# Optimization experiments

Hardware: AMD Instinct MI355X
Metric: run time of the kernel (lower is better)

## Reference

```python
import jax, jax.numpy as jnp
import numpy as np

N = 50000      # num_nodes
E = 500000     # num_edges
D_IN = 128     # in_features
D_OUT = 128    # out_features
D_REL = 128    # nrela_dim
NEG_SLOPE = 0.2   # LeakyReLU alpha
RATIO = 0.5       # float ratio -> simple (non-schedule) branch
LN_EPS = 1e-5


def setup_inputs() -> dict:
    key = jax.random.key(0)
    ks = jax.random.split(key, 8)
    edge_index = jax.random.randint(ks[0], (2, E), 0, N, dtype=jnp.int64)
    x = jax.random.normal(ks[1], (N, D_IN), dtype=jnp.float32)
    edge_type_embed = jax.random.normal(ks[2], (E, D_REL), dtype=jnp.float32)
    # learned params (xavier-ish scale)
    W = jax.random.normal(ks[3], (4, 2 * D_OUT + D_REL, D_OUT), dtype=jnp.float32) * 0.05
    a = jax.random.normal(ks[4], (4, D_OUT, 1), dtype=jnp.float32) * 0.05
    xw = jax.random.normal(ks[5], (D_IN, D_OUT), dtype=jnp.float32) * (1.0 / np.sqrt(D_IN))
    xb = jnp.zeros((D_OUT,), dtype=jnp.float32)
    gamma = jnp.ones((D_OUT,), dtype=jnp.float32)
    beta = jnp.zeros((D_OUT,), dtype=jnp.float32)
    return {"edge_index": edge_index, "x": x, "edge_type_embed": edge_type_embed,
            "W": W, "a": a, "xw": xw, "xb": xb, "gamma": gamma, "beta": beta}


def _segment_softmax(score, seg, num_segments):
    # per-source-node softmax over edges (matches torch_geometric softmax util)
    seg_max = jax.ops.segment_max(score, seg, num_segments=num_segments)
    seg_max = jnp.where(jnp.isfinite(seg_max), seg_max, 0.0)  # empty segments
    e = jnp.exp(score - seg_max[seg])
    denom = jax.ops.segment_sum(e, seg, num_segments=num_segments)
    return e / (denom[seg] + 1e-16)


def _one_iter(edge_index, xc, ete, Wi, ai):
    src, dst = edge_index[0], edge_index[1]
    # [E, 2*D_OUT + D_REL] @ [2*D_OUT+D_REL, D_OUT] -> [E, D_OUT]
    edge_h = jnp.concatenate([xc[src], xc[dst], ete], axis=1) @ Wi
    score = jax.nn.leaky_relu(jnp.squeeze(edge_h @ ai, -1), NEG_SLOPE)  # [E]
    alpha = _segment_softmax(score, src, N)
    k = int(E * RATIO)
    _, idx = jax.lax.top_k(alpha, k)
    mask = jnp.zeros((E,), dtype=bool).at[idx].set(True)
    alpha = jnp.where(mask, alpha, 0.0)
    # scatter-add weighted messages back to source nodes
    return jax.ops.segment_sum(alpha[:, None] * edge_h, src, num_segments=N)


def reference(edge_index, x, edge_type_embed, W, a, xw, xb, gamma, beta):
    xc = x @ xw + xb  # x_linear
    for i in range(4):  # fixed 4 aggregation iterations (float-ratio branch)
        xc = _one_iter(edge_index, xc, edge_type_embed, W[i], a[i])
    xc = jax.nn.elu(xc)  # concat=True
    mu = jnp.mean(xc, axis=-1, keepdims=True)
    var = jnp.var(xc, axis=-1, keepdims=True)
    return (xc - mu) * jax.lax.rsqrt(var + LN_EPS) * gamma + beta
```

## Files before the change

### kernel.cpp

```cpp
#include <hip/hip_runtime.h>
#include <math.h>

#define DOUT 128

typedef unsigned short u16;
typedef __attribute__((ext_vector_type(8))) short bf16x8;
typedef __attribute__((ext_vector_type(4))) float f32x4;

static __device__ __forceinline__ f32x4 mfma16x16x32(bf16x8 a, bf16x8 b, f32x4 c) {
  return __builtin_amdgcn_mfma_f32_16x16x32_bf16(a, b, c, 0, 0, 0);
}

static __device__ __forceinline__ short bf16i(int v) {
  return (short)(__float_as_uint((float)v) >> 16);
}

static __device__ __forceinline__ float wsum64(float v) {
#pragma unroll
  for (int off = 32; off > 0; off >>= 1) v += __shfl_xor(v, off, 64);
  return v;
}
static __device__ __forceinline__ float wmax64(float v) {
#pragma unroll
  for (int off = 32; off > 0; off >>= 1) v = fmaxf(v, __shfl_xor(v, off, 64));
  return v;
}
static __device__ __forceinline__ float rsumg(float v) {
  v += __shfl_xor(v, 16, 64);
  v += __shfl_xor(v, 32, 64);
  return v;
}

static __device__ __forceinline__ void split3(float x, u16& h, u16& m, u16& l) {
  unsigned u = __float_as_uint(x);
  unsigned rh = u + 0x7FFFu + ((u >> 16) & 1u);
  h = (u16)(rh >> 16);
  float hf = __uint_as_float(rh & 0xFFFF0000u);
  float d1 = x - hf;
  unsigned v = __float_as_uint(d1);
  unsigned rm = v + 0x7FFFu + ((v >> 16) & 1u);
  m = (u16)(rm >> 16);
  float mf = __uint_as_float(rm & 0xFFFF0000u);
  float d2 = d1 - mf;
  unsigned w2 = __float_as_uint(d2);
  unsigned rl = w2 + 0x7FFFu + ((w2 >> 16) & 1u);
  l = (u16)(rl >> 16);
}

static __device__ __forceinline__ void split3pk(float x0, float x1,
                                                unsigned& h, unsigned& m, unsigned& l) {
  unsigned hp, mp, lp;
  asm("v_cvt_pk_bf16_f32 %0, %1, %2" : "=v"(hp) : "v"(x0), "v"(x1));
  float d0 = x0 - __uint_as_float(hp << 16);
  float d1 = x1 - __uint_as_float(hp & 0xFFFF0000u);
  asm("v_cvt_pk_bf16_f32 %0, %1, %2" : "=v"(mp) : "v"(d0), "v"(d1));
  float e0 = d0 - __uint_as_float(mp << 16);
  float e1 = d1 - __uint_as_float(mp & 0xFFFF0000u);
  asm("v_cvt_pk_bf16_f32 %0, %1, %2" : "=v"(lp) : "v"(e0), "v"(e1));
  h = hp; m = mp; l = lp;
}
static __device__ __forceinline__ void split34pk(float4 v, uint2& h, uint2& m, uint2& lo) {
  split3pk(v.x, v.y, h.x, m.x, lo.x);
  split3pk(v.z, v.w, h.y, m.y, lo.y);
}

__global__ void zero_detect_kernel(int* __restrict__ degcur, unsigned* __restrict__ hists,
                                   unsigned* __restrict__ rep, int* __restrict__ candcnt4,
                                   int N, const void* __restrict__ ei, int* __restrict__ flag,
                                   int E) {
  int i = blockIdx.x * blockDim.x + threadIdx.x;
  if (i < N) degcur[i] = 0;
  if (i < 4096) hists[i] = 0u;
  if (i < 32768) rep[i] = 0u;
  if (i < 4) candcnt4[i] = 0;
  const int* p = (const int*)ei;
  int lim = (E < 65536) ? E : 65536;
  int any = 0;
  for (int j = i; j < lim; j += gridDim.x * blockDim.x) any |= (p[2 * j + 1] != 0);
  if (__any(any))
    if ((threadIdx.x & 63) == 0 && any) atomicOr(flag, 1);
}

__global__ void cvt_deg_kernel(const void* __restrict__ ei, const int* __restrict__ flag,
                               int* __restrict__ src, int* __restrict__ dst,
                               int* __restrict__ degcur, int E) {
  int i = blockIdx.x * blockDim.x + threadIdx.x;
  if (i >= E) return;
  int s, d;
  if (*flag) { const int* p = (const int*)ei; s = p[i]; d = p[E + i]; }
  else { const long long* p = (const long long*)ei; s = (int)p[i]; d = (int)p[(size_t)E + i]; }
  src[i] = s;
  dst[i] = d;
  atomicAdd(&degcur[s], 1);
}

__global__ void scan_rowptr_kernel(int* __restrict__ degcur, int* __restrict__ rowptr, int N) {
  const int tid = threadIdx.x;
  const int lane = tid & 63, wid = tid >> 6;
  __shared__ int wsumS[16];
  __shared__ int sbase;
  if (tid == 0) sbase = 0;
  __syncthreads();
  for (int base = 0; base < N; base += 1024) {
    int i = base + tid;
    int v = (i < N) ? degcur[i] : 0;
    int x = v;
#pragma unroll
    for (int off = 1; off < 64; off <<= 1) {
      int y = __shfl_up(x, off, 64);
      if (lane >= off) x += y;
    }
    if (lane == 63) wsumS[wid] = x;
    __syncthreads();
    int wbase = 0;
#pragma unroll
    for (int w2 = 0; w2 < 16; ++w2) wbase += (w2 < wid) ? wsumS[w2] : 0;
    int excl = sbase + wbase + x - v;
    if (i < N) { rowptr[i] = excl; degcur[i] = excl; }
    __syncthreads();
    if (tid == 1023) sbase += wbase + x;
    __syncthreads();
  }
  if (tid == 0) rowptr[N] = sbase;
}

__global__ void scatter_kernel(const int* __restrict__ src, int* __restrict__ cursor,
                               int* __restrict__ eids, int E) {
  int e = blockIdx.x * blockDim.x + threadIdx.x;
  if (e >= E) return;
  int p = atomicAdd(&cursor[src[e]], 1);
  eids[p] = e;
}

__global__ void sort_eids_kernel(const int* __restrict__ rowptr, int* __restrict__ eids, int N) {
  int n = blockIdx.x * blockDim.x + threadIdx.x;
  if (n >= N) return;
  int p0 = rowptr[n], p1 = rowptr[n + 1];
  for (int i = p0 + 1; i < p1; ++i) {
    int key = eids[i];
    int j = i - 1;
    while (j >= p0 && eids[j] > key) { eids[j + 1] = eids[j]; --j; }
    eids[j + 1] = key;
  }
}

__global__ void wprep_kernel(const float* __restrict__ W, const float* __restrict__ a,
                             float* __restrict__ wa_all, const float* __restrict__ xw,
                             u16* __restrict__ wtH, u16* __restrict__ wtM,
                             u16* __restrict__ wtL) {
  int blk = blockIdx.x;
  int tid = threadIdx.x;
  if (blk < 4) {
    int it = blk, k = tid;
    const float* row = W + ((size_t)it * 384 + k) * DOUT;
    const float* ai = a + (size_t)it * DOUT;
    float acc = 0.f;
    for (int j = 0; j < DOUT; ++j) acc = fmaf(row[j], ai[j], acc);
    wa_all[it * 384 + k] = acc;
    return;
  }
  __shared__ int muS[32];
  {
    int lw = tid & 63, g = lw >> 4;
    bf16x8 aEnc;
#pragma unroll
    for (int j = 0; j < 8; ++j) aEnc[j] = bf16i(8 * g + j + 1);
    f32x4 z = {0.f, 0.f, 0.f, 0.f};
    for (int t0 = 0; t0 < 32; ++t0) {
      int g0 = t0 >> 3, j0 = t0 & 7;
      bf16x8 bOne;
#pragma unroll
      for (int j = 0; j < 8; ++j)
        bOne[j] = (g == g0 && j == j0) ? (short)0x3F80 : (short)0;
      f32x4 d = mfma16x16x32(aEnc, bOne, z);
      if (tid == t0) muS[t0] = ((int)(d[0] + 0.5f) - 1) & 31;
    }
  }
  __syncthreads();
  int b = blk - 4;
  int set, ks;
  const float* srcp;
  if (b < 4) { set = 0; ks = b; srcp = xw; }
  else { set = 1 + (b - 4) / 12; ks = (b - 4) % 12; srcp = W + (size_t)(set - 1) * 384 * DOUT; }
  size_t base = ((size_t)set * 12 + ks) * 4096;
  for (int i = tid; i < 4096; i += blockDim.x) {
    int col = i >> 5, t = i & 31;
    float x = srcp[(size_t)(ks * 32 + muS[t]) * DOUT + col];
    u16 h, m, l;
    split3(x, h, m, l);
    wtH[base + i] = h;
    wtM[base + i] = m;
    wtL[base + i] = l;
  }
}

__global__ __launch_bounds__(256) void et4_kernel(const float* __restrict__ ete,
                                                  const float* __restrict__ wa_all,
                                                  float* __restrict__ et4, int E) {
  __shared__ float4 w3s[4][32];
  int tid = threadIdx.x;
  if (tid < 128) {
    int it = tid >> 5, k4 = tid & 31;
    const float* base = wa_all + it * 384 + 256 + k4 * 4;
    w3s[it][k4] = make_float4(base[0], base[1], base[2], base[3]);
  }
  __syncthreads();
  int e = blockIdx.x * blockDim.x + tid;
  if (e >= E) return;
  const float4* row = (const float4*)(ete + (size_t)e * DOUT);
  float a0 = 0.f, a1 = 0.f, a2 = 0.f, a3 = 0.f;
#pragma unroll
  for (int k4 = 0; k4 < 32; ++k4) {
    float4 r = row[k4];
    float4 w0 = w3s[0][k4], w1 = w3s[1][k4], w2 = w3s[2][k4], w3v = w3s[3][k4];
    a0 = fmaf(r.x, w0.x, fmaf(r.y, w0.y, fmaf(r.z, w0.z, fmaf(r.w, w0.w, a0))));
    a1 = fmaf(r.x, w1.x, fmaf(r.y, w1.y, fmaf(r.z, w1.z, fmaf(r.w, w1.w, a1))));
    a2 = fmaf(r.x, w2.x, fmaf(r.y, w2.y, fmaf(r.z, w2.z, fmaf(r.w, w2.w, a2))));
    a3 = fmaf(r.x, w3v.x, fmaf(r.y, w3v.y, fmaf(r.z, w3v.z, fmaf(r.w, w3v.w, a3))));
  }
  et4[e] = a0;
  et4[(size_t)E + e] = a1;
  et4[(size_t)2 * E + e] = a2;
  et4[(size_t)3 * E + e] = a3;
}

__global__ __launch_bounds__(256) void softmax_kernel(
    const int* __restrict__ rowptr, const int* __restrict__ eids, const int* __restrict__ dst,
    const float* __restrict__ pa, const float* __restrict__ qa, const float* __restrict__ et4,
    int it, int E, float* __restrict__ alpha, unsigned* __restrict__ rep0, int N) {
  __shared__ unsigned lh[256];
  int tid = threadIdx.x;
  lh[tid] = 0u;
  __syncthreads();
  const float* etp = et4 + (size_t)it * E;
  int w = (int)(((size_t)blockIdx.x * blockDim.x + tid) >> 6);
  int lane = tid & 63;
  if (w < N) {
    int p0 = rowptr[w], p1 = rowptr[w + 1];
    int deg = p1 - p0;
    if (deg > 0) {
      float pan = pa[w];
      if (deg <= 64) {
        int p = p0 + lane;
        int e = -1;
        float sv = -3.402823466e38f;
        if (p < p1) {
          e = eids[p];
          float s = pan + qa[dst[e]] + etp[e];
          sv = (s >= 0.f) ? s : 0.2f * s;
        }
        float m = wmax64(sv);
        float ee = (e >= 0) ? expf(sv - m) : 0.f;
        float den = 0.f;
        for (int i = 0; i < deg; ++i) den += __shfl(ee, i, 64);
        den += 1e-16f;
        if (e >= 0) {
          float av = ee / den;
          alpha[e] = av;
          atomicAdd(&lh[__float_as_uint(av) >> 24], 1u);
        }
      } else if (deg <= 256) {
        float sv[4]; int ev[4];
#pragma unroll
        for (int u = 0; u < 4; ++u) {
          int p = p0 + u * 64 + lane;
          if (p < p1) {
            int e = eids[p];
            ev[u] = e;
            float s = pan + qa[dst[e]] + etp[e];
            sv[u] = (s >= 0.f) ? s : 0.2f * s;
          } else { ev[u] = -1; sv[u] = -3.402823466e38f; }
        }
        float m = fmaxf(fmaxf(sv[0], sv[1]), fmaxf(sv[2], sv[3]));
        m = wmax64(m);
        float ssum = 0.f;
#pragma unroll
        for (int u = 0; u < 4; ++u)
          if (ev[u] >= 0) { sv[u] = expf(sv[u] - m); ssum += sv[u]; }
        ssum = wsum64(ssum);
        float den = ssum + 1e-16f;
#pragma unroll
        for (int u = 0; u < 4; ++u)
          if (ev[u] >= 0) {
            float av = sv[u] / den;
            alpha[ev[u]] = av;
            atomicAdd(&lh[__float_as_uint(av) >> 24], 1u);
          }
      } else {
        float m = -3.402823466e38f;
        for (int p = p0 + lane; p < p1; p += 64) {
          int e = eids[p];
          float s = pan + qa[dst[e]] + etp[e];
          s = (s >= 0.f) ? s : 0.2f * s;
          m = fmaxf(m, s);
        }
        m = wmax64(m);
        float ssum = 0.f;
        for (int p = p0 + lane; p < p1; p += 64) {
          int e = eids[p];
          float s = pan + qa[dst[e]] + etp[e];
          s = (s >= 0.f) ? s : 0.2f * s;
          ssum += expf(s - m);
        }
        ssum = wsum64(ssum);
        float den = ssum + 1e-16f;
        for (int p = p0 + lane; p < p1; p += 64) {
          int e = eids[p];
          float s = pan + qa[dst[e]] + etp[e];
          s = (s >= 0.f) ? s : 0.2f * s;
          float av = expf(s - m) / den;
          alpha[e] = av;
          atomicAdd(&lh[__float_as_uint(av) >> 24], 1u);
        }
      }
    }
  }
  __syncthreads();
  if (lh[tid]) atomicAdd(&rep0[(blockIdx.x & 31) * 256 + tid], lh[tid]);
}

__device__ __forceinline__ void scan256_step(const unsigned* __restrict__ hist, unsigned krem_in,
                                             unsigned* lds, unsigned* res,
                                             unsigned& bin, unsigned& krem_out) {
  int t = threadIdx.x;
  if (t < 256) lds[t] = hist[t];
  __syncthreads();
  for (int off = 1; off < 256; off <<= 1) {
    unsigned add = 0u;
    if (t < 256 && t + off < 256) add = lds[t + off];
    __syncthreads();
    if (t < 256) lds[t] += add;
    __syncthreads();
  }
  if (t < 256) {
    unsigned above = (t == 255) ? 0u : lds[t + 1];
    if (lds[t] >= krem_in && above < krem_in) { res[0] = (unsigned)t; res[1] = krem_in - above; }
  }
  __syncthreads();
  bin = res[0];
  krem_out = res[1];
  __syncthreads();
}

__device__ __forceinline__ void chain_scan(const unsigned* __restrict__ hists, int upto,
                                           unsigned Ktop, unsigned* lds, unsigned* res,
                                           unsigned& pref, unsigned& krem) {
  pref = 0u; krem = Ktop;
  for (int l = 0; l < upto; ++l) {
    unsigned bin, k2;
    scan256_step(hists + l * 256, krem, lds, res, bin, k2);
    pref |= bin << (24 - 8 * l);
    krem = k2;
  }
}

__global__ __launch_bounds__(256) void hist1_kernel(const float* __restrict__ alpha,
                                                    const unsigned* __restrict__ rep0,
                                                    unsigned* __restrict__ hists_it,
                                                    unsigned Ktop, int E) {
  __shared__ unsigned lds[256], res2[2], lh[256];
  int t = threadIdx.x;
  unsigned v = 0u;
#pragma unroll
  for (int r = 0; r < 32; ++r) v += rep0[r * 256 + t];
  if (blockIdx.x == 0) hists_it[t] = v;
  lds[t] = v;
  __syncthreads();
  for (int off = 1; off < 256; off <<= 1) {
    unsigned add = (t + off < 256) ? lds[t + off] : 0u;
    __syncthreads();
    lds[t] += add;
    __syncthreads();
  }
  {
    unsigned above = (t == 255) ? 0u : lds[t + 1];
    if (lds[t] >= Ktop && above < Ktop) { res2[0] = (unsigned)t; res2[1] = Ktop - above; }
  }
  __syncthreads();
  unsigned bin0 = res2[0];
  lh[t] = 0u;
  __syncthreads();
  unsigned* myh = hists_it + 256;
  for (int e = blockIdx.x * blockDim.x + t; e < E; e += gridDim.x * blockDim.x) {
    unsigned b = __float_as_uint(alpha[e]);
    if ((b >> 24) == bin0) atomicAdd(&lh[(b >> 16) & 0xFFu], 1u);
  }
  __syncthreads();
  if (lh[t]) atomicAdd(&myh[t], lh[t]);
}

__global__ void hist_kernel(const float* __restrict__ alpha, unsigned* __restrict__ hists_it,
                            int level, unsigned Ktop, int E) {
  __shared__ unsigned lds[256], res2[2], lh[256];
  unsigned pref = 0u, krem = Ktop;
  if (level > 0) chain_scan(hists_it, level, Ktop, lds, res2, pref, krem);
  int t = threadIdx.x;
  lh[t] = 0u;
  __syncthreads();
  unsigned* myh = hists_it + level * 256;
  int hs = (level > 0) ? (32 - 8 * level) : 0;
  int bs = 24 - 8 * level;
  for (int e = blockIdx.x * blockDim.x + t; e < E; e += gridDim.x * blockDim.x) {
    unsigned b = __float_as_uint(alpha[e]);
    if (level == 0 || (b >> hs) == (pref >> hs)) atomicAdd(&lh[(b >> bs) & 0xFFu], 1u);
  }
  __syncthreads();
  if (lh[t]) atomicAdd(&myh[t], lh[t]);
}

__global__ void hist3c_kernel(const float* __restrict__ alpha, unsigned* __restrict__ hists_it,
                              unsigned Ktop, int* __restrict__ candList,
                              int* __restrict__ candCnt, int E) {
  __shared__ unsigned lds[256], res2[2], lh[256];
  unsigned pref, krem;
  chain_scan(hists_it, 3, Ktop, lds, res2, pref, krem);
  int t = threadIdx.x;
  lh[t] = 0u;
  __syncthreads();
  unsigned* myh = hists_it + 3 * 256;
  for (int e = blockIdx.x * blockDim.x + t; e < E; e += gridDim.x * blockDim.x) {
    unsigned b = __float_as_uint(alpha[e]);
    if ((b >> 8) == (pref >> 8)) {
      atomicAdd(&lh[b & 0xFFu], 1u);
      int p = atomicAdd(candCnt, 1);
      if (p < 4096) candList[p] = e;
    }
  }
  __syncthreads();
  if (lh[t]) atomicAdd(&myh[t], lh[t]);
}

__global__ __launch_bounds__(1024) void resolve24_kernel(
    const float* __restrict__ alpha, float* __restrict__ amask,
    const unsigned* __restrict__ hists_it, unsigned Ktop,
    const int* __restrict__ candList, const int* __restrict__ candCnt,
    int* __restrict__ header, int E) {
  __shared__ unsigned lds[256], res2[2];
  unsigned thr, needU;
  chain_scan(hists_it, 4, Ktop, lds, res2, thr, needU);
  int needT = (int)needU;
  int cc = *candCnt;
  int tid = threadIdx.x;
  __shared__ int tiel[4096];
  __shared__ int tiec;
  if (tid == 0) tiec = 0;
  __syncthreads();
  if (cc <= 4096) {
    for (int i = tid; i < cc; i += blockDim.x) {
      int e = candList[i];
      if (__float_as_uint(alpha[e]) == thr) { int p = atomicAdd(&tiec, 1); tiel[p] = e; }
    }
    __syncthreads();
    int ce = tiec;
    int dropc = ce - needT;
    if (dropc <= 0) {
      if (tid == 0) { header[0] = 0; header[1] = (int)thr; header[2] = 0; }
      return;
    }
    if (dropc <= 64) {
      int sortN = 64;
      while (sortN < ce) sortN <<= 1;
      for (int i = tid; i < sortN; i += blockDim.x)
        if (i >= ce) tiel[i] = 0x7fffffff;
      __syncthreads();
      for (int k = 2; k <= sortN; k <<= 1) {
        for (int j = k >> 1; j > 0; j >>= 1) {
          for (int i = tid; i < sortN; i += blockDim.x) {
            int ixj = i ^ j;
            if (ixj > i) {
              int v0 = tiel[i], v1 = tiel[ixj];
              bool up = ((i & k) == 0);
              if ((v0 > v1) == up) { tiel[i] = v1; tiel[ixj] = v0; }
            }
          }
          __syncthreads();
        }
      }
      if (tid == 0) { header[0] = 0; header[1] = (int)thr; header[2] = dropc; }
      for (int i = tid; i < dropc; i += blockDim.x) header[3 + i] = tiel[needT + i];
      return;
    }
  }
  if (tid == 0) { header[0] = 1; }
  __shared__ int wtot[16];
  __shared__ int sbase;
  if (tid == 0) sbase = 0;
  __syncthreads();
  int lane = tid & 63, wid = tid >> 6;
  for (int base = 0; base < E; base += 1024) {
    int e = base + tid;
    float a = 0.f; int f = 0; unsigned b = 0u;
    if (e < E) { a = alpha[e]; b = __float_as_uint(a); f = (b == thr) ? 1 : 0; }
    int x = f;
#pragma unroll
    for (int off = 1; off < 64; off <<= 1) {
      int y = __shfl_up(x, off, 64);
      if (lane >= off) x += y;
    }
    if (lane == 63) wtot[wid] = x;
    __syncthreads();
    int wbase = 0;
#pragma unroll
    for (int w2 = 0; w2 < 16; ++w2) wbase += (w2 < wid) ? wtot[w2] : 0;
    if (e < E) {
      float outv = 0.f;
      if (b > thr) outv = a;
      else if (f && (sbase + wbase + x - f) < needT) outv = a;
      amask[e] = outv;
    }
    __syncthreads();
    if (tid == 1023) sbase += wbase + x;
    __syncthreads();
  }
}

static __device__ __forceinline__ float edge_w(const float* __restrict__ alpha,
                                               const float* __restrict__ amask,
                                               const int* __restrict__ hdr, int flg,
                                               unsigned thr, int dc, int e) {
  if (flg) return amask[e];
  float av = alpha[e];
  unsigned b = __float_as_uint(av);
  if (b > thr) return av;
  if (b == thr) {
    for (int j = 0; j < dc; ++j)
      if (hdr[3 + j] == e) return 0.f;
    return av;
  }
  return 0.f;
}

__global__ void agg_kernel(const int* __restrict__ rowptr, const int* __restrict__ eids,
                           const int* __restrict__ dst, const float* __restrict__ alpha,
                           const float* __restrict__ amask, const int* __restrict__ hdr,
                           const float* __restrict__ xc, const float* __restrict__ ete,
                           float* __restrict__ sa, float* __restrict__ vbuf,
                           float* __restrict__ tbuf, int N) {
  int w = (int)(((size_t)blockIdx.x * blockDim.x + threadIdx.x) >> 6);
  int lane = threadIdx.x & 63;
  if (w >= N) return;
  const int flg = hdr[0];
  const unsigned thr = (unsigned)hdr[1];
  const int dc = hdr[2];
  int p0 = rowptr[w], p1 = rowptr[w + 1];
  int deg = p1 - p0;
  const int half = lane >> 5;
  const int l32 = lane & 31;
  const float4* xc4 = (const float4*)xc;
  const float4* et4p = (const float4*)ete;
  float4 acc = make_float4(0.f, 0.f, 0.f, 0.f);
  float s = 0.f;
  if (deg <= 64) {
    int p = p0 + lane;
    int e = -1; float am = 0.f; int dd = 0;
    if (p < p1) { e = eids[p]; am = edge_w(alpha, amask, hdr, flg, thr, dc, e); dd = dst[e]; }
    for (int i = 0; i < deg; ++i) {
      float a = __shfl(am, i, 64);
      if (a != 0.f) {
        int ei = __shfl(e, i, 64);
        int di = __shfl(dd, i, 64);
        const float4* b = half ? (et4p + (size_t)ei * 32) : (xc4 + (size_t)di * 32);
        float4 r = b[l32];
        acc.x = fmaf(a, r.x, acc.x); acc.y = fmaf(a, r.y, acc.y);
        acc.z = fmaf(a, r.z, acc.z); acc.w = fmaf(a, r.w, acc.w);
        s += a;
      }
    }
  } else {
    for (int p = p0; p < p1; ++p) {
      int e0 = eids[p];
      float a0 = edge_w(alpha, amask, hdr, flg, thr, dc, e0);
      if (a0 != 0.f) {
        int d0 = dst[e0];
        const float4* b0 = half ? (et4p + (size_t)e0 * 32) : (xc4 + (size_t)d0 * 32);
        float4 r = b0[l32];
        acc.x = fmaf(a0, r.x, acc.x); acc.y = fmaf(a0, r.y, acc.y);
        acc.z = fmaf(a0, r.z, acc.z); acc.w = fmaf(a0, r.w, acc.w);
        s += a0;
      }
    }
  }
  if (half == 0) ((float4*)vbuf)[(size_t)w * 32 + l32] = acc;
  else           ((float4*)tbuf)[(size_t)w * 32 + l32] = acc;
  if (lane == 0) sa[w] = s;
}

__global__ __launch_bounds__(256) void gemm_mfma_kernel(
    const float* __restrict__ A0, const float* __restrict__ A1, const float* __restrict__ A2,
    const float* __restrict__ sca, const u16* __restrict__ wtH, const u16* __restrict__ wtM,
    const u16* __restrict__ wtL, const float* __restrict__ bias, float* __restrict__ C,
    int N, int nseg,
    const float* __restrict__ wa_next, float* __restrict__ pa, float* __restrict__ qa,
    const float* __restrict__ gamma, const float* __restrict__ beta,
    float* __restrict__ outp, int epi) {
  __shared__ __align__(16) char smem[61440];
  u16 (*AsH)[40] = (u16(*)[40])(smem);
  u16 (*AsM)[40] = (u16(*)[40])(smem + 10240);
  u16 (*AsL)[40] = (u16(*)[40])(smem + 20480);
  u16 (*BsH)[40] = (u16(*)[40])(smem + 30720);
  u16 (*BsM)[40] = (u16(*)[40])(smem + 40960);
  u16 (*BsL)[40] = (u16(*)[40])(smem + 51200);
  const int tid = threadIdx.x;
  const int m0 = blockIdx.x * 128;
  const int K = DOUT * nseg;
  const int w = tid >> 6, l = tid & 63;
  const int cb = l & 15, g = l >> 4;

  int rowlab[4], collab[4];
  {
    bf16x8 enc, ones;
#pragma unroll
    for (int j = 0; j < 8; ++j) { enc[j] = bf16i(cb + 1); ones[j] = (short)0x3F80; }
    f32x4 z = {0.f, 0.f, 0.f, 0.f};
    f32x4 dR = mfma16x16x32(enc, ones, z);
    f32x4 dC = mfma16x16x32(ones, enc, z);
#pragma unroll
    for (int r = 0; r < 4; ++r) {
      rowlab[r] = ((int)(dR[r] * (1.f / 32.f) + 0.5f) - 1) & 15;
      collab[r] = ((int)(dC[r] * (1.f / 32.f) + 0.5f) - 1) & 15;
    }
  }

  f32x4 acc[2][8];
#pragma unroll
  for (int i = 0; i < 2; ++i)
#pragma unroll
    for (int j = 0; j < 8; ++j) acc[i][j] = (f32x4){0.f, 0.f, 0.f, 0.f};

  const int srow = tid >> 1, shalf = tid & 1;
  const int grow_s = m0 + srow;
  float scv = 1.f;
  if (sca && grow_s < N) scv = sca[grow_s];

  auto loadA = [&](int kc, float4& v0, float4& v1, float4& v2, float4& v3) {
    const int seg = kc >> 7;
    const float* Ap = (seg == 0) ? A0 : (seg == 1) ? A1 : A2;
    v0 = make_float4(0.f, 0.f, 0.f, 0.f); v1 = v0; v2 = v0; v3 = v0;
    if (grow_s < N) {
      const float4* p = (const float4*)(Ap + (size_t)grow_s * DOUT + (kc & 127) + shalf * 16);
      v0 = p[0]; v1 = p[1]; v2 = p[2]; v3 = p[3];
      if (seg == 0 && sca) {
        v0.x *= scv; v0.y *= scv; v0.z *= scv; v0.w *= scv;
        v1.x *= scv; v1.y *= scv; v1.z *= scv; v1.w *= scv;
        v2.x *= scv; v2.y *= scv; v2.z *= scv; v2.w *= scv;
        v3.x *= scv; v3.y *= scv; v3.z *= scv; v3.w *= scv;
      }
    }
  };
  auto loadB = [&](int kc, uint4& h0, uint4& h1, uint4& m0u, uint4& m1u, uint4& l0u,
                   uint4& l1u) {
    size_t sb = (size_t)(kc >> 5) << 12;
    const uint4* gh = (const uint4*)(wtH + sb) + tid * 2;
    const uint4* gm = (const uint4*)(wtM + sb) + tid * 2;
    const uint4* gl = (const uint4*)(wtL + sb) + tid * 2;
    h0 = gh[0]; h1 = gh[1];
    m0u = gm[0]; m1u = gm[1];
    l0u = gl[0]; l1u = gl[1];
  };

  float4 av0, av1, av2, av3, nv0, nv1, nv2, nv3;
  uint4 bh0, bh1, bm0u, bm1u, bl0u, bl1u, nh0, nh1, nm0, nm1, nl0, nl1;
  loadA(0, av0, av1, av2, av3);
  loadB(0, bh0, bh1, bm0u, bm1u, bl0u, bl1u);

  const int nks = K >> 5;
  for (int ks = 0; ks < nks; ++ks) {
    const int kc = ks << 5;
    {
      uint2 h0, m0v, l0, h1, m1v, l1, h2, m2v, l2, h3, m3v, l3;
      split34pk(av0, h0, m0v, l0); split34pk(av1, h1, m1v, l1);
      split34pk(av2, h2, m2v, l2); split34pk(av3, h3, m3v, l3);
      *(uint4*)&AsH[srow][shalf * 16]     = make_uint4(h0.x, h0.y, h1.x, h1.y);
      *(uint4*)&AsH[srow][shalf * 16 + 8] = make_uint4(h2.x, h2.y, h3.x, h3.y);
      *(uint4*)&AsM[srow][shalf * 16]     = make_uint4(m0v.x, m0v.y, m1v.x, m1v.y);
      *(uint4*)&AsM[srow][shalf * 16 + 8] = make_uint4(m2v.x, m2v.y, m3v.x, m3v.y);
      *(uint4*)&AsL[srow][shalf * 16]     = make_uint4(l0.x, l0.y, l1.x, l1.y);
      *(uint4*)&AsL[srow][shalf * 16 + 8] = make_uint4(l2.x, l2.y, l3.x, l3.y);
      *(uint4*)&BsH[srow][shalf * 16]     = bh0;
      *(uint4*)&BsH[srow][shalf * 16 + 8] = bh1;
      *(uint4*)&BsM[srow][shalf * 16]     = bm0u;
      *(uint4*)&BsM[srow][shalf * 16 + 8] = bm1u;
      *(uint4*)&BsL[srow][shalf * 16]     = bl0u;
      *(uint4*)&BsL[srow][shalf * 16 + 8] = bl1u;
    }
    if (ks + 1 < nks) {
      loadA(kc + 32, nv0, nv1, nv2, nv3);
      loadB(kc + 32, nh0, nh1, nm0, nm1, nl0, nl1);
    }
    __syncthreads();
    bf16x8 aH0 = *(const bf16x8*)&AsH[w * 32 + cb][g * 8];
    bf16x8 aH1 = *(const bf16x8*)&AsH[w * 32 + 16 + cb][g * 8];
    bf16x8 aM0 = *(const bf16x8*)&AsM[w * 32 + cb][g * 8];
    bf16x8 aM1 = *(const bf16x8*)&AsM[w * 32 + 16 + cb][g * 8];
    bf16x8 aL0 = *(const bf16x8*)&AsL[w * 32 + cb][g * 8];
    bf16x8 aL1 = *(const bf16x8*)&AsL[w * 32 + 16 + cb][g * 8];
#pragma unroll
    for (int ct = 0; ct < 8; ++ct) {
      bf16x8 bH = *(const bf16x8*)&BsH[ct * 16 + cb][g * 8];
      bf16x8 bM = *(const bf16x8*)&BsM[ct * 16 + cb][g * 8];
      bf16x8 bL = *(const bf16x8*)&BsL[ct * 16 + cb][g * 8];
      acc[0][ct] = mfma16x16x32(aH0, bH, acc[0][ct]);
      acc[1][ct] = mfma16x16x32(aH1, bH, acc[1][ct]);
      acc[0][ct] = mfma16x16x32(aM0, bH, acc[0][ct]);
      acc[1][ct] = mfma16x16x32(aM1, bH, acc[1][ct]);
      acc[0][ct] = mfma16x16x32(aL0, bH, acc[0][ct]);
      acc[1][ct] = mfma16x16x32(aL1, bH, acc[1][ct]);
      acc[0][ct] = mfma16x16x32(aH0, bM, acc[0][ct]);
      acc[1][ct] = mfma16x16x32(aH1, bM, acc[1][ct]);
      acc[0][ct] = mfma16x16x32(aM0, bM, acc[0][ct]);
      acc[1][ct] = mfma16x16x32(aM1, bM, acc[1][ct]);
      acc[0][ct] = mfma16x16x32(aH0, bL, acc[0][ct]);
      acc[1][ct] = mfma16x16x32(aH1, bL, acc[1][ct]);
    }
    __syncthreads();
    av0 = nv0; av1 = nv1; av2 = nv2; av3 = nv3;
    bh0 = nh0; bh1 = nh1; bm0u = nm0; bm1u = nm1; bl0u = nl0; bl1u = nl1;
  }

  float* slab = (float*)(smem + (size_t)w * 8448);
  const int row16 = l & 15;
  const int csel = (l >> 4) * 32;
#pragma unroll
  for (int rt = 0; rt < 2; ++rt) {
#pragma unroll
    for (int ct = 0; ct < 8; ++ct)
#pragma unroll
      for (int r = 0; r < 4; ++r)
        slab[rowlab[r] * 132 + ct * 16 + collab[r]] = acc[rt][ct][r];
    __syncthreads();
    int grow = m0 + w * 32 + rt * 16 + row16;
    float v[32];
#pragma unroll
    for (int q = 0; q < 8; ++q) {
      float4 t4 = *(float4*)&slab[row16 * 132 + csel + q * 4];
      v[q * 4 + 0] = t4.x; v[q * 4 + 1] = t4.y; v[q * 4 + 2] = t4.z; v[q * 4 + 3] = t4.w;
    }
    if (bias) {
#pragma unroll
      for (int q = 0; q < 8; ++q) {
        float4 bb = *(const float4*)(bias + csel + q * 4);
        v[q * 4 + 0] += bb.x; v[q * 4 + 1] += bb.y; v[q * 4 + 2] += bb.z; v[q * 4 + 3] += bb.w;
      }
    }
    if (epi == 2) {
#pragma unroll
      for (int i = 0; i < 32; ++i) v[i] = (v[i] > 0.f) ? v[i] : expm1f(v[i]);
      float s = 0.f;
#pragma unroll
      for (int i = 0; i < 32; ++i) s += v[i];
      s = rsumg(s);
      float mu = s * (1.f / 128.f);
      float sq = 0.f;
#pragma unroll
      for (int i = 0; i < 32; ++i) { float d = v[i] - mu; sq += d * d; }
      sq = rsumg(sq);
      float rstd = rsqrtf(sq * (1.f / 128.f) + 1e-5f);
      if (grow < N) {
#pragma unroll
        for (int q = 0; q < 8; ++q) {
          float4 ga = *(const float4*)(gamma + csel + q * 4);
          float4 be = *(const float4*)(beta + csel + q * 4);
          float4 o;
          o.x = (v[q * 4 + 0] - mu) * rstd * ga.x + be.x;
          o.y = (v[q * 4 + 1] - mu) * rstd * ga.y + be.y;
          o.z = (v[q * 4 + 2] - mu) * rstd * ga.z + be.z;
          o.w = (v[q * 4 + 3] - mu) * rstd * ga.w + be.w;
          *(float4*)(outp + (size_t)grow * DOUT + csel + q * 4) = o;
        }
      }
    } else {
      if (grow < N) {
#pragma unroll
        for (int q = 0; q < 8; ++q)
          *(float4*)(C + (size_t)grow * DOUT + csel + q * 4) =
              make_float4(v[q * 4 + 0], v[q * 4 + 1], v[q * 4 + 2], v[q * 4 + 3]);
      }
      if (epi == 1) {
        float pp = 0.f, qq = 0.f;
#pragma unroll
        for (int i = 0; i < 32; ++i) {
          pp = fmaf(v[i], wa_next[csel + i], pp);
          qq = fmaf(v[i], wa_next[128 + csel + i], qq);
        }
        pp = rsumg(pp);
        qq = rsumg(qq);
        if ((l >> 4) == 0 && grow < N) { pa[grow] = pp; qa[grow] = qq; }
      }
    }
    __syncthreads();
  }
}

extern "C" void kernel_launch(void* const* d_in, const int* in_sizes, int n_in,
                              void* d_out, int out_size, void* d_ws, size_t ws_size,
                              hipStream_t stream) {
  const int E = in_sizes[0] / 2;
  const int N = in_sizes[1] / DOUT;
  const unsigned Ktop = (unsigned)(E / 2);

  const void*  ei    = d_in[0];
  const float* x     = (const float*)d_in[1];
  const float* ete   = (const float*)d_in[2];
  const float* W     = (const float*)d_in[3];
  const float* a     = (const float*)d_in[4];
  const float* xw    = (const float*)d_in[5];
  const float* xb    = (const float*)d_in[6];
  const float* gamma = (const float*)d_in[7];
  const float* beta  = (const float*)d_in[8];
  float* out = (float*)d_out;

  size_t off = 0;
  auto take = [&](size_t bytes) -> char* {
    char* p = (char*)d_ws + off;
    off += (bytes + 255) & ~(size_t)255;
    return p;
  };
  int*      src32   = (int*)take((size_t)E * 4);
  int*      dst32   = (int*)take((size_t)E * 4);
  int*      rowptr  = (int*)take(((size_t)N + 1) * 4);
  int*      degcur  = (int*)take((size_t)N * 4);
  int*      eids    = (int*)take((size_t)E * 4);
  float*    pa      = (float*)take((size_t)N * 4);
  float*    qa      = (float*)take((size_t)N * 4);
  float*    wa_all  = (float*)take(4 * 384 * 4);
  float*    alpha   = (float*)take((size_t)E * 4);
  float*    amask   = (float*)take((size_t)E * 4);
  float*    sa      = (float*)take((size_t)N * 4);
  float*    vbuf    = (float*)take((size_t)N * DOUT * 4);
  float*    tbuf    = (float*)take((size_t)N * DOUT * 4);
  float*    xcA     = (float*)take((size_t)N * DOUT * 4);
  float*    xcB     = (float*)take((size_t)N * DOUT * 4);
  float*    et4     = (float*)take((size_t)E * 4 * 4);
  unsigned* hists   = (unsigned*)take(4 * 4 * 256 * 4);
  unsigned* rep     = (unsigned*)take(4 * 32 * 256 * 4);
  int*      candcnt4= (int*)take(64);
  int*      flag    = (int*)take(64);
  int*      candList= (int*)take(4096 * 4);
  int*      header  = (int*)take(4 * 80 * 4);
  u16*      wtH     = (u16*)take((size_t)5 * 12 * 4096 * 2);
  u16*      wtM     = (u16*)take((size_t)5 * 12 * 4096 * 2);
  u16*      wtL     = (u16*)take((size_t)5 * 12 * 4096 * 2);
  (void)ws_size; (void)n_in; (void)out_size;

  const int TB  = 256;
  const int gE  = (E + TB - 1) / TB;
  const int gN  = (N + TB - 1) / TB;
  const int gN4 = (N + 3) / 4;
  const int gM  = (N + 127) / 128;

  (void)hipMemsetAsync(flag, 0, 4, stream);
  zero_detect_kernel<<<gN, TB, 0, stream>>>(degcur, hists, rep, candcnt4, N, ei, flag, E);
  cvt_deg_kernel<<<gE, TB, 0, stream>>>(ei, flag, src32, dst32, degcur, E);
  scan_rowptr_kernel<<<1, 1024, 0, stream>>>(degcur, rowptr, N);
  scatter_kernel<<<gE, TB, 0, stream>>>(src32, degcur, eids, E);
  sort_eids_kernel<<<gN, TB, 0, stream>>>(rowptr, eids, N);
  wprep_kernel<<<56, 384, 0, stream>>>(W, a, wa_all, xw, wtH, wtM, wtL);
  et4_kernel<<<gE, TB, 0, stream>>>(ete, wa_all, et4, E);
  gemm_mfma_kernel<<<gM, 256, 0, stream>>>(x, nullptr, nullptr, nullptr, wtH, wtM, wtL, xb,
                                           xcA, N, 1, wa_all, pa, qa, nullptr, nullptr,
                                           nullptr, 1);

  float* bufs[2] = {xcA, xcB};
  for (int it = 0; it < 4; ++it) {
    const float* xc = bufs[it & 1];
    float* xn = bufs[(it & 1) ^ 1];
    unsigned* hists_it = hists + it * 1024;
    unsigned* rep_it = rep + it * 8192;
    int* hdr_it = header + it * 80;
    const u16* wH = wtH + (size_t)(it + 1) * 12 * 4096;
    const u16* wM = wtM + (size_t)(it + 1) * 12 * 4096;
    const u16* wL = wtL + (size_t)(it + 1) * 12 * 4096;

    softmax_kernel<<<gN4, TB, 0, stream>>>(rowptr, eids, dst32, pa, qa, et4, it, E, alpha,
                                           rep_it, N);
    hist1_kernel<<<384, 256, 0, stream>>>(alpha, rep_it, hists_it, Ktop, E);
    hist_kernel<<<384, 256, 0, stream>>>(alpha, hists_it, 2, Ktop, E);
    hist3c_kernel<<<384, 256, 0, stream>>>(alpha, hists_it, Ktop, candList,
                                           candcnt4 + it, E);
    resolve24_kernel<<<1, 1024, 0, stream>>>(alpha, amask, hists_it, Ktop, candList,
                                             candcnt4 + it, hdr_it, E);
    agg_kernel<<<gN4, TB, 0, stream>>>(rowptr, eids, dst32, alpha, amask, hdr_it,
                                       xc, ete, sa, vbuf, tbuf, N);
    if (it < 3)
      gemm_mfma_kernel<<<gM, 256, 0, stream>>>(xc, vbuf, tbuf, sa, wH, wM, wL, nullptr, xn,
                                               N, 3, wa_all + (it + 1) * 384, pa, qa,
                                               nullptr, nullptr, nullptr, 1);
    else
      gemm_mfma_kernel<<<gM, 256, 0, stream>>>(xc, vbuf, tbuf, sa, wH, wM, wL, nullptr, xn,
                                               N, 3, nullptr, pa, qa, gamma, beta, out, 2);
  }
}
```

Before: 884.0 us.

## Fuse radix-select histogram passes and resolve into one kernel with grid barriers

Merges the three histogram kernels and the single-block resolve kernel of the top-k radix select into one persistent 384-block kernel. Software grid barriers built on atomic counters replace the kernel boundaries, so each block no longer re-runs the chained prefix scans of earlier levels. The final resolve runs on block 0 with 256 threads instead of 1024. This cuts three launches per iteration and the redundant scans, but depends on all 384 blocks being co-resident to avoid deadlock, and the slow fallback path now uses fewer threads.

```diff
diff --git a/kernel.cpp b/kernel.cpp
--- a/kernel.cpp
+++ b/kernel.cpp
@@ -64,15 +64,27 @@
   split3pk(v.z, v.w, h.y, m.y, lo.y);
 }
 
+static __device__ __forceinline__ void gbar(int* ctr, int nb) {
+  __threadfence();
+  __syncthreads();
+  if (threadIdx.x == 0) {
+    atomicAdd(ctr, 1);
+    while (atomicAdd(ctr, 0) < nb) __builtin_amdgcn_s_sleep(4);
+  }
+  __syncthreads();
+  __threadfence();
+}
+
 __global__ void zero_detect_kernel(int* __restrict__ degcur, unsigned* __restrict__ hists,
                                    unsigned* __restrict__ rep, int* __restrict__ candcnt4,
-                                   int N, const void* __restrict__ ei, int* __restrict__ flag,
-                                   int E) {
+                                   int* __restrict__ bar, int N, const void* __restrict__ ei,
+                                   int* __restrict__ flag, int E) {
   int i = blockIdx.x * blockDim.x + threadIdx.x;
   if (i < N) degcur[i] = 0;
   if (i < 4096) hists[i] = 0u;
   if (i < 32768) rep[i] = 0u;
   if (i < 4) candcnt4[i] = 0;
+  if (i < 16) bar[i] = 0;
   const int* p = (const int*)ei;
   int lim = (E < 65536) ? E : 65536;
   int any = 0;
@@ -319,17 +331,16 @@
   if (lh[tid]) atomicAdd(&rep0[(blockIdx.x & 31) * 256 + tid], lh[tid]);
 }
 
-__device__ __forceinline__ void scan256_step(const unsigned* __restrict__ hist, unsigned krem_in,
-                                             unsigned* lds, unsigned* res,
-                                             unsigned& bin, unsigned& krem_out) {
+__device__ __forceinline__ void scan256g(unsigned* __restrict__ hist, unsigned krem_in,
+                                         unsigned* lds, unsigned* res,
+                                         unsigned& bin, unsigned& krem_out) {
   int t = threadIdx.x;
-  if (t < 256) lds[t] = hist[t];
+  lds[t] = atomicAdd(&hist[t], 0u);
   __syncthreads();
   for (int off = 1; off < 256; off <<= 1) {
-    unsigned add = 0u;
-    if (t < 256 && t + off < 256) add = lds[t + off];
-    __syncthreads();
-    if (t < 256) lds[t] += add;
+    unsigned add = (t + off < 256) ? lds[t + off] : 0u;
+    __syncthreads();
+    lds[t] += add;
     __syncthreads();
   }
   if (t < 256) {
@@ -342,28 +353,20 @@
   __syncthreads();
 }
 
-__device__ __forceinline__ void chain_scan(const unsigned* __restrict__ hists, int upto,
-                                           unsigned Ktop, unsigned* lds, unsigned* res,
-                                           unsigned& pref, unsigned& krem) {
-  pref = 0u; krem = Ktop;
-  for (int l = 0; l < upto; ++l) {
-    unsigned bin, k2;
-    scan256_step(hists + l * 256, krem, lds, res, bin, k2);
-    pref |= bin << (24 - 8 * l);
-    krem = k2;
-  }
-}
-
-__global__ __launch_bounds__(256) void hist1_kernel(const float* __restrict__ alpha,
-                                                    const unsigned* __restrict__ rep0,
-                                                    unsigned* __restrict__ hists_it,
-                                                    unsigned Ktop, int E) {
+__global__ __launch_bounds__(256) void select_kernel(
+    const float* __restrict__ alpha, const unsigned* __restrict__ rep0,
+    unsigned* __restrict__ hists_it, unsigned Ktop,
+    int* __restrict__ candList, int* __restrict__ candCnt,
+    int* __restrict__ header, float* __restrict__ amask, int E, int* __restrict__ bar) {
   __shared__ unsigned lds[256], res2[2], lh[256];
-  int t = threadIdx.x;
+  __shared__ int tiel[4096];
+  __shared__ int tiec;
+  const int t = threadIdx.x;
+  const int nb = (int)gridDim.x;
+  const int stride = nb * 256;
   unsigned v = 0u;
 #pragma unroll
   for (int r = 0; r < 32; ++r) v += rep0[r * 256 + t];
-  if (blockIdx.x == 0) hists_it[t] = v;
   lds[t] = v;
   __syncthreads();
   for (int off = 1; off < 256; off <<= 1) {
@@ -377,76 +380,64 @@
     if (lds[t] >= Ktop && above < Ktop) { res2[0] = (unsigned)t; res2[1] = Ktop - above; }
   }
   __syncthreads();
-  unsigned bin0 = res2[0];
+  unsigned bin0 = res2[0], krem = res2[1];
+  __syncthreads();
   lh[t] = 0u;
   __syncthreads();
-  unsigned* myh = hists_it + 256;
-  for (int e = blockIdx.x * blockDim.x + t; e < E; e += gridDim.x * blockDim.x) {
+  for (int e = blockIdx.x * 256 + t; e < E; e += stride) {
     unsigned b = __float_as_uint(alpha[e]);
     if ((b >> 24) == bin0) atomicAdd(&lh[(b >> 16) & 0xFFu], 1u);
   }
   __syncthreads();
-  if (lh[t]) atomicAdd(&myh[t], lh[t]);
-}
-
-__global__ void hist_kernel(const float* __restrict__ alpha, unsigned* __restrict__ hists_it,
-                            int level, unsigned Ktop, int E) {
-  __shared__ unsigned lds[256], res2[2], lh[256];
-  unsigned pref = 0u, krem = Ktop;
-  if (level > 0) chain_scan(hists_it, level, Ktop, lds, res2, pref, krem);
-  int t = threadIdx.x;
+  if (lh[t]) atomicAdd(&hists_it[256 + t], lh[t]);
+  gbar(bar + 0, nb);
+  unsigned bin1, k2;
+  scan256g(hists_it + 256, krem, lds, res2, bin1, k2);
+  krem = k2;
+  unsigned pref16 = (bin0 << 8) | bin1;
   lh[t] = 0u;
   __syncthreads();
-  unsigned* myh = hists_it + level * 256;
-  int hs = (level > 0) ? (32 - 8 * level) : 0;
-  int bs = 24 - 8 * level;
-  for (int e = blockIdx.x * blockDim.x + t; e < E; e += gridDim.x * blockDim.x) {
+  for (int e = blockIdx.x * 256 + t; e < E; e += stride) {
     unsigned b = __float_as_uint(alpha[e]);
-    if (level == 0 || (b >> hs) == (pref >> hs)) atomicAdd(&lh[(b >> bs) & 0xFFu], 1u);
-  }
-  __syncthreads();
-  if (lh[t]) atomicAdd(&myh[t], lh[t]);
-}
-
-__global__ void hist3c_kernel(const float* __restrict__ alpha, unsigned* __restrict__ hists_it,
-                              unsigned Ktop, int* __restrict__ candList,
-                              int* __restrict__ candCnt, int E) {
-  __shared__ unsigned lds[256], res2[2], lh[256];
-  unsigned pref, krem;
-  chain_scan(hists_it, 3, Ktop, lds, res2, pref, krem);
-  int t = threadIdx.x;
+    if ((b >> 16) == pref16) atomicAdd(&lh[(b >> 8) & 0xFFu], 1u);
+  }
+  __syncthreads();
+  if (lh[t]) atomicAdd(&hists_it[512 + t], lh[t]);
+  gbar(bar + 1, nb);
+  unsigned bin2;
+  scan256g(hists_it + 512, krem, lds, res2, bin2, k2);
+  krem = k2;
+  unsigned pref24 = (pref16 << 8) | bin2;
   lh[t] = 0u;
   __syncthreads();
-  unsigned* myh = hists_it + 3 * 256;
-  for (int e = blockIdx.x * blockDim.x + t; e < E; e += gridDim.x * blockDim.x) {
+  for (int e = blockIdx.x * 256 + t; e < E; e += stride) {
     unsigned b = __float_as_uint(alpha[e]);
-    if ((b >> 8) == (pref >> 8)) {
+    if ((b >> 8) == pref24) {
       atomicAdd(&lh[b & 0xFFu], 1u);
       int p = atomicAdd(candCnt, 1);
       if (p < 4096) candList[p] = e;
     }
   }
   __syncthreads();
-  if (lh[t]) atomicAdd(&myh[t], lh[t]);
-}
-
-__global__ __launch_bounds__(1024) void resolve24_kernel(
-    const float* __restrict__ alpha, float* __restrict__ amask,
-    const unsigned* __restrict__ hists_it, unsigned Ktop,
-    const int* __restrict__ candList, const int* __restrict__ candCnt,
-    int* __restrict__ header, int E) {
-  __shared__ unsigned lds[256], res2[2];
-  unsigned thr, needU;
-  chain_scan(hists_it, 4, Ktop, lds, res2, thr, needU);
+  if (lh[t]) atomicAdd(&hists_it[768 + t], lh[t]);
+  __threadfence();
+  __syncthreads();
+  if (t == 0) atomicAdd(bar + 2, 1);
+  if (blockIdx.x != 0) return;
+  if (t == 0) {
+    while (atomicAdd(bar + 2, 0) < nb) __builtin_amdgcn_s_sleep(4);
+  }
+  __syncthreads();
+  __threadfence();
+  unsigned bin3, needU;
+  scan256g(hists_it + 768, krem, lds, res2, bin3, needU);
+  unsigned thr = (pref24 << 8) | bin3;
   int needT = (int)needU;
-  int cc = *candCnt;
-  int tid = threadIdx.x;
-  __shared__ int tiel[4096];
-  __shared__ int tiec;
-  if (tid == 0) tiec = 0;
+  int cc = atomicAdd(candCnt, 0);
+  if (t == 0) tiec = 0;
   __syncthreads();
   if (cc <= 4096) {
-    for (int i = tid; i < cc; i += blockDim.x) {
+    for (int i = t; i < cc; i += blockDim.x) {
       int e = candList[i];
       if (__float_as_uint(alpha[e]) == thr) { int p = atomicAdd(&tiec, 1); tiel[p] = e; }
     }
@@ -454,18 +445,18 @@
     int ce = tiec;
     int dropc = ce - needT;
     if (dropc <= 0) {
-      if (tid == 0) { header[0] = 0; header[1] = (int)thr; header[2] = 0; }
+      if (t == 0) { header[0] = 0; header[1] = (int)thr; header[2] = 0; }
       return;
     }
     if (dropc <= 64) {
       int sortN = 64;
       while (sortN < ce) sortN <<= 1;
-      for (int i = tid; i < sortN; i += blockDim.x)
+      for (int i = t; i < sortN; i += blockDim.x)
         if (i >= ce) tiel[i] = 0x7fffffff;
       __syncthreads();
       for (int k = 2; k <= sortN; k <<= 1) {
         for (int j = k >> 1; j > 0; j >>= 1) {
-          for (int i = tid; i < sortN; i += blockDim.x) {
+          for (int i = t; i < sortN; i += blockDim.x) {
             int ixj = i ^ j;
             if (ixj > i) {
               int v0 = tiel[i], v1 = tiel[ixj];
@@ -476,19 +467,19 @@
           __syncthreads();
         }
       }
-      if (tid == 0) { header[0] = 0; header[1] = (int)thr; header[2] = dropc; }
-      for (int i = tid; i < dropc; i += blockDim.x) header[3 + i] = tiel[needT + i];
+      if (t == 0) { header[0] = 0; header[1] = (int)thr; header[2] = dropc; }
+      for (int i = t; i < dropc; i += blockDim.x) header[3 + i] = tiel[needT + i];
       return;
     }
   }
-  if (tid == 0) { header[0] = 1; }
-  __shared__ int wtot[16];
+  if (t == 0) header[0] = 1;
+  __shared__ int wtot4[4];
   __shared__ int sbase;
-  if (tid == 0) sbase = 0;
-  __syncthreads();
-  int lane = tid & 63, wid = tid >> 6;
-  for (int base = 0; base < E; base += 1024) {
-    int e = base + tid;
+  if (t == 0) sbase = 0;
+  __syncthreads();
+  int lane = t & 63, wid = t >> 6;
+  for (int base = 0; base < E; base += 256) {
+    int e = base + t;
     float a = 0.f; int f = 0; unsigned b = 0u;
     if (e < E) { a = alpha[e]; b = __float_as_uint(a); f = (b == thr) ? 1 : 0; }
     int x = f;
@@ -497,11 +488,11 @@
       int y = __shfl_up(x, off, 64);
       if (lane >= off) x += y;
     }
-    if (lane == 63) wtot[wid] = x;
+    if (lane == 63) wtot4[wid] = x;
     __syncthreads();
     int wbase = 0;
 #pragma unroll
-    for (int w2 = 0; w2 < 16; ++w2) wbase += (w2 < wid) ? wtot[w2] : 0;
+    for (int w2 = 0; w2 < 4; ++w2) wbase += (w2 < wid) ? wtot4[w2] : 0;
     if (e < E) {
       float outv = 0.f;
       if (b > thr) outv = a;
@@ -509,7 +500,7 @@
       amask[e] = outv;
     }
     __syncthreads();
-    if (tid == 1023) sbase += wbase + x;
+    if (t == 255) sbase += wbase + x;
     __syncthreads();
   }
 }
@@ -840,6 +831,7 @@
   u16*      wtH     = (u16*)take((size_t)5 * 12 * 4096 * 2);
   u16*      wtM     = (u16*)take((size_t)5 * 12 * 4096 * 2);
   u16*      wtL     = (u16*)take((size_t)5 * 12 * 4096 * 2);
+  int*      bar     = (int*)take(64);
   (void)ws_size; (void)n_in; (void)out_size;
 
   const int TB  = 256;
@@ -849,7 +841,7 @@
   const int gM  = (N + 127) / 128;
 
   (void)hipMemsetAsync(flag, 0, 4, stream);
-  zero_detect_kernel<<<gN, TB, 0, stream>>>(degcur, hists, rep, candcnt4, N, ei, flag, E);
+  zero_detect_kernel<<<gN, TB, 0, stream>>>(degcur, hists, rep, candcnt4, bar, N, ei, flag, E);
   cvt_deg_kernel<<<gE, TB, 0, stream>>>(ei, flag, src32, dst32, degcur, E);
   scan_rowptr_kernel<<<1, 1024, 0, stream>>>(degcur, rowptr, N);
   scatter_kernel<<<gE, TB, 0, stream>>>(src32, degcur, eids, E);
@@ -873,12 +865,8 @@
 
     softmax_kernel<<<gN4, TB, 0, stream>>>(rowptr, eids, dst32, pa, qa, et4, it, E, alpha,
                                            rep_it, N);
-    hist1_kernel<<<384, 256, 0, stream>>>(alpha, rep_it, hists_it, Ktop, E);
-    hist_kernel<<<384, 256, 0, stream>>>(alpha, hists_it, 2, Ktop, E);
-    hist3c_kernel<<<384, 256, 0, stream>>>(alpha, hists_it, Ktop, candList,
-                                           candcnt4 + it, E);
-    resolve24_kernel<<<1, 1024, 0, stream>>>(alpha, amask, hists_it, Ktop, candList,
-                                             candcnt4 + it, hdr_it, E);
+    select_kernel<<<384, 256, 0, stream>>>(alpha, rep_it, hists_it, Ktop, candList,
+                                           candcnt4 + it, hdr_it, amask, E, bar + it * 3);
     agg_kernel<<<gN4, TB, 0, stream>>>(rowptr, eids, dst32, alpha, amask, hdr_it,
                                        xc, ete, sa, vbuf, tbuf, N);
     if (it < 3)
```

After: 1.399 ms. +58.3%, slower.
